# Kernel tuning notes

Hardware: AMD Instinct MI355X
Metric: run time of the kernel (lower is better)

The kernel has to match this reference:

```python
import jax, jax.numpy as jnp
import numpy as np
from jax import lax

B, N_PROP, N_GT = 8, 8000, 256
NUM_CLASSES = 2
IMG_H = IMG_W = 800.0
FG_T = BG_T = 0.5            # Matcher thresholds
WX, WY, WW, WH = 10.0, 10.0, 5.0, 5.0  # BoxCoder weights
SCORE_T, NMS_T = 0.05, 0.5
PRE_NMS, DETS = 1000, 300     # boxes entering NMS, detections_per_img
DW_CLIP = float(np.log(1000.0 / 16.0))


def _rand_boxes(key, shape):
    k1, k2, k3, k4 = jax.random.split(key, 4)
    x1 = jax.random.uniform(k1, shape) * (IMG_W - 60.0)
    y1 = jax.random.uniform(k2, shape) * (IMG_H - 60.0)
    w = 10.0 + jax.random.uniform(k3, shape) * 250.0
    h = 10.0 + jax.random.uniform(k4, shape) * 250.0
    return jnp.stack([x1, y1, jnp.minimum(x1 + w, IMG_W), jnp.minimum(y1 + h, IMG_H)], -1)


def setup_inputs() -> dict:
    key = jax.random.key(0)
    kp, kg, kl, kb = jax.random.split(key, 4)
    n_all = N_PROP + N_GT
    return {
        "proposals": _rand_boxes(kp, (B, N_PROP)),
        "gt_boxes": _rand_boxes(kg, (B, N_GT)),
        "logits": jax.random.normal(kl, (B, n_all, NUM_CLASSES), jnp.float32),
        "box_regression": jax.random.normal(kb, (B, n_all, NUM_CLASSES * 4), jnp.float32) * 0.1,
    }


def box_iou(a, b):
    # a: [Na,4], b: [Nb,4] in xyxy -> [Na,Nb]
    area_a = (a[:, 2] - a[:, 0]) * (a[:, 3] - a[:, 1])
    area_b = (b[:, 2] - b[:, 0]) * (b[:, 3] - b[:, 1])
    lt = jnp.maximum(a[:, None, :2], b[None, :, :2])
    rb = jnp.minimum(a[:, None, 2:], b[None, :, 2:])
    wh = jnp.clip(rb - lt, 0.0)
    inter = wh[..., 0] * wh[..., 1]
    return inter / (area_a[:, None] + area_b[None, :] - inter)


def encode(ref_boxes, gt):
    # BoxCoder.encode, weights (10,10,5,5)
    pw = ref_boxes[:, 2] - ref_boxes[:, 0]
    ph = ref_boxes[:, 3] - ref_boxes[:, 1]
    pcx = ref_boxes[:, 0] + 0.5 * pw
    pcy = ref_boxes[:, 1] + 0.5 * ph
    gw = gt[:, 2] - gt[:, 0]
    gh = gt[:, 3] - gt[:, 1]
    gcx = gt[:, 0] + 0.5 * gw
    gcy = gt[:, 1] + 0.5 * gh
    return jnp.stack([
        WX * (gcx - pcx) / pw,
        WY * (gcy - pcy) / ph,
        WW * jnp.log(gw / pw),
        WH * jnp.log(gh / ph),
    ], -1)


def decode(rel, boxes):
    # rel: [N, C*4], boxes: [N,4] -> [N, C, 4]
    rel = rel.reshape(rel.shape[0], -1, 4)
    pw = boxes[:, 2] - boxes[:, 0]
    ph = boxes[:, 3] - boxes[:, 1]
    pcx = boxes[:, 0] + 0.5 * pw
    pcy = boxes[:, 1] + 0.5 * ph
    dx = rel[..., 0] / WX
    dy = rel[..., 1] / WY
    dw = jnp.minimum(rel[..., 2] / WW, DW_CLIP)
    dh = jnp.minimum(rel[..., 3] / WH, DW_CLIP)
    cx = dx * pw[:, None] + pcx[:, None]
    cy = dy * ph[:, None] + pcy[:, None]
    w = jnp.exp(dw) * pw[:, None]
    h = jnp.exp(dh) * ph[:, None]
    return jnp.stack([cx - 0.5 * w, cy - 0.5 * h, cx + 0.5 * w, cy + 0.5 * h], -1)


def _per_image(prop, gt, logit, breg):
    n_all = prop.shape[0] + gt.shape[0]
    prop_all = jnp.concatenate([prop, gt], 0)  # select_training_samples concat

    # --- assign_targets_to_proposals (Matcher) ---
    iou = box_iou(gt, prop_all)                 # [G, N_all]
    vals = iou.max(0)
    matches = iou.argmax(0)
    # gt_labels are all 1; bg -> 0, between thresholds -> -1 (empty when fg==bg)
    labels = jnp.where(vals < BG_T, 0, jnp.where(vals < FG_T, -1, 1))
    matched_gt = gt[matches]                    # [N_all, 4]
    reg_targets = encode(prop_all, matched_gt)  # [N_all, 4]

    # --- postprocess_detections ---
    pred = decode(breg, prop_all)               # [N_all, C, 4]
    boxes1 = pred[:, 1, :]                      # drop background class
    boxes1 = jnp.stack([
        jnp.clip(boxes1[:, 0], 0.0, IMG_W),
        jnp.clip(boxes1[:, 1], 0.0, IMG_H),
        jnp.clip(boxes1[:, 2], 0.0, IMG_W),
        jnp.clip(boxes1[:, 3], 0.0, IMG_H),
    ], -1)
    scores = jax.nn.softmax(logit, -1)[:, 1]
    sc = jnp.where(scores > SCORE_T, scores, -1.0)  # score_thresh filter

    top_s, top_i = lax.top_k(sc, PRE_NMS)
    top_b = boxes1[top_i]                       # [M, 4]
    ious = box_iou(top_b, top_b)                # [M, M]
    idx = jnp.arange(PRE_NMS)

    def body(keep, i):
        sup = (ious[i] > NMS_T) & keep[i] & (idx > i)
        return keep & ~sup, None

    keep, _ = lax.scan(body, jnp.ones(PRE_NMS, bool), idx)
    final = jnp.where(keep & (top_s > 0.0), top_s, -1.0)
    det_s, sel = lax.top_k(final, DETS)
    det_b = top_b[sel]
    return labels.astype(jnp.float32), reg_targets, det_b, det_s


def reference(proposals, gt_boxes, logits, box_regression):
    return jax.vmap(_per_image)(proposals, gt_boxes, logits, box_regression)
```

## Files before the change

### kernel.cpp

```cpp
#include <hip/hip_runtime.h>
#include <math.h>

#pragma clang fp contract(off)

#define BATCH 8
#define N_PROP 8000
#define N_GT 256
#define N_ALL 8256
#define PRE_NMS 1000
#define DETS 300
#define IMG 800.0f
#define DW_CLIP 4.135166556742356f
#define NWORDS 32
#define NBINS 8192
#define BIN_SCALE 8192.0f
#define PREP_PER_BATCH 65
#define SEL_BLOCKS 8

__device__ __forceinline__ float exf(float x) { return (float)exp((double)x); }
__device__ __forceinline__ float lgf(float x) { return (float)log((double)x); }

__device__ __forceinline__ int score_bin(float s) {
  int b = (int)(s * BIN_SCALE);
  return (b < 0) ? 0 : (b > NBINS - 1 ? NBINS - 1 : b);
}

__device__ __forceinline__ int bxp(int j) { return j ^ ((j >> 5) & 7); }

#define REP32(F) F(0) F(1) F(2) F(3) F(4) F(5) F(6) F(7) F(8) F(9) F(10) \
  F(11) F(12) F(13) F(14) F(15) F(16) F(17) F(18) F(19) F(20) F(21) F(22) \
  F(23) F(24) F(25) F(26) F(27) F(28) F(29) F(30) F(31)


__global__ void __launch_bounds__(1024)
fused_select_prep_kernel(const float* __restrict__ prop,
                         const float* __restrict__ gt,
                         const float* __restrict__ logits,
                         const float* __restrict__ breg,
                         float* __restrict__ out_labels,
                         float* __restrict__ out_regt,
                         float* __restrict__ top_s,
                         float* __restrict__ top_b) {
  const int idx = blockIdx.x;
  const int tid = threadIdx.x;
  __shared__ __align__(16) float ssc[N_ALL];
  __shared__ unsigned hist[NBINS];
  __shared__ __align__(16) float sc2[N_ALL];
  __shared__ unsigned short idx2[N_ALL];
  __shared__ __align__(16) float4 gsh[N_GT];
  __shared__ int s_wt[16], s_wx[16];
  __shared__ int s_T, s_Nc;
  __shared__ __align__(16) float4 gsh4[N_GT];
  __shared__ float s_best[128];
  __shared__ int s_bi[128];

  if (idx < SEL_BLOCKS) {
    const int b = idx;
    const int lane = tid & 63, wid = tid >> 6;

    if (tid < N_GT) gsh[tid] = ((const float4*)(gt + (size_t)b * N_GT * 4))[tid];

    for (int k = tid; k < N_ALL; k += 1024) {
      const float2 lg = *(const float2*)(logits + ((size_t)b * N_ALL + k) * 2);
      const float m = fmaxf(lg.x, lg.y);
      const float e0 = exf(lg.x - m), e1 = exf(lg.y - m);
      const float s = e1 / (e0 + e1);
      ssc[k] = (s > 0.05f) ? s : -1.0f;
    }
    #pragma unroll
    for (int i = 0; i < NBINS / 1024; ++i) hist[tid + i * 1024] = 0u;
    __syncthreads();
    for (int k = tid; k < N_ALL; k += 1024)
      atomicAdd(&hist[score_bin(ssc[k])], 1u);
    __syncthreads();

    int local = 0;
    #pragma unroll
    for (int i = 0; i < NBINS / 1024; ++i) local += (int)hist[tid * (NBINS / 1024) + i];

    int incl = local;
    #pragma unroll
    for (int off = 1; off < 64; off <<= 1) {
      const int u = __shfl_down(incl, off);
      incl += (lane + off < 64) ? u : 0;
    }
    if (lane == 0) s_wt[wid] = incl;
    __syncthreads();
    if (tid < 16) {
      const int v = s_wt[tid];
      int inc2 = v;
      #pragma unroll
      for (int off = 1; off < 16; off <<= 1) {
        const int u = __shfl_down(inc2, off);
        inc2 += (tid + off < 16) ? u : 0;
      }
      s_wx[tid] = inc2 - v;
    }
    __syncthreads();
    const int sa = (incl - local) + s_wx[wid];

    {
      int above = sa;
      const int hi = tid * (NBINS / 1024) + (NBINS / 1024) - 1;
      #pragma unroll
      for (int i = 0; i < NBINS / 1024; ++i) {
        const int bin = hi - i;
        const int c = (int)hist[bin];
        if (above < PRE_NMS && above + c >= PRE_NMS) { s_T = bin; s_Nc = above + c; }
        hist[bin] = (unsigned)above;
        above += c;
      }
    }
    __syncthreads();
    const int T = s_T;
    const int Nc = s_Nc;

    for (int k = tid; k < N_ALL; k += 1024) {
      const float v = ssc[k];
      const int bb = score_bin(v);
      if (bb >= T) {
        const int slot = (int)atomicAdd(&hist[bb], 1u);
        sc2[slot] = v;
        idx2[slot] = (unsigned short)k;
      }
    }
    __syncthreads();

    float* tsb = top_s + (size_t)b * PRE_NMS;
    float4* tbb = (float4*)top_b + (size_t)b * PRE_NMS;
    for (int s = tid; s < Nc; s += 1024) {
      const float my = sc2[s];
      const int myb = score_bin(my);
      const int myi = (int)idx2[s];
      int gl = s;
      while (gl > 0 && score_bin(sc2[gl - 1]) == myb) --gl;
      int rank = gl;
      for (int k2 = gl; k2 < Nc; ++k2) {
        const float v = sc2[k2];
        if (score_bin(v) != myb) break;
        if (k2 == s) continue;
        rank += (int)((v > my) | ((v == my) & ((int)idx2[k2] < myi)));
      }
      if (rank < PRE_NMS) {
        tsb[rank] = my;
        float4 pb;
        if (myi < N_PROP) pb = ((const float4*)(prop + (size_t)b * N_PROP * 4))[myi];
        else              pb = gsh[myi - N_PROP];
        const float pw = pb.z - pb.x, ph = pb.w - pb.y;
        const float pcx = pb.x + 0.5f * pw, pcy = pb.y + 0.5f * ph;
        const float4 r = *(const float4*)(breg + (((size_t)b * N_ALL + myi) * 8 + 4));
        const float dx = r.x / 10.0f, dy = r.y / 10.0f;
        const float dw = fminf(r.z / 5.0f, DW_CLIP);
        const float dh = fminf(r.w / 5.0f, DW_CLIP);
        const float cx = dx * pw + pcx, cy = dy * ph + pcy;
        const float w2 = exf(dw) * pw, h2 = exf(dh) * ph;
        float4 bb;
        bb.x = fminf(fmaxf(cx - 0.5f * w2, 0.0f), IMG);
        bb.y = fminf(fmaxf(cy - 0.5f * h2, 0.0f), IMG);
        bb.z = fminf(fmaxf(cx + 0.5f * w2, 0.0f), IMG);
        bb.w = fminf(fmaxf(cy + 0.5f * h2, 0.0f), IMG);
        tbb[rank] = bb;
      }
    }
  } else {
    const int pbx = idx - SEL_BLOCKS;
    const int b = pbx / PREP_PER_BATCH;
    const int blk = pbx - b * PREP_PER_BATCH;
    {
      if (tid < N_GT)
        gsh4[tid] = ((const float4*)(gt + (size_t)b * N_GT * 4))[tid];
    }
    __syncthreads();

    const int grp = tid >> 3;
    const int gl  = tid & 7;
    const int j0b = blk * 128;
    const int j = j0b + grp;
    const bool jv = (j < N_ALL);

    float x1, y1, x2, y2;
    if (jv && j < N_PROP) {
      const float4 p = ((const float4*)(prop + (size_t)b * N_PROP * 4))[j];
      x1 = p.x; y1 = p.y; x2 = p.z; y2 = p.w;
    } else if (jv) {
      const float4 g = gsh4[j - N_PROP];
      x1 = g.x; y1 = g.y; x2 = g.z; y2 = g.w;
    } else {
      const float4 g = gsh4[0];
      x1 = g.x; y1 = g.y; x2 = g.z; y2 = g.w;
    }
    const float areaP = (x2 - x1) * (y2 - y1);

    float best = -1.0f; int bi = gl;
    #pragma unroll 4
    for (int t = 0; t < 32; ++t) {
      const int i = gl + (t << 3);
      const float4 g = gsh4[i];
      const float ga = (g.z - g.x) * (g.w - g.y);
      const float w = fmaxf(fminf(g.z, x2) - fmaxf(g.x, x1), 0.0f);
      const float h = fmaxf(fminf(g.w, y2) - fmaxf(g.y, y1), 0.0f);
      const float inter = w * h;
      const float iou = inter / (ga + areaP - inter);
      if (iou > best) { best = iou; bi = i; }
    }
    #pragma unroll
    for (int m = 1; m < 8; m <<= 1) {
      const float ov = __shfl_xor(best, m, 64);
      const int   oi = __shfl_xor(bi,  m, 64);
      if (ov > best || (ov == best && oi < bi)) { best = ov; bi = oi; }
    }
    if (gl == 0) { s_best[grp] = best; s_bi[grp] = bi; }
    __syncthreads();

    if (tid < 128) {
      const int j2 = j0b + tid;
      if (j2 < N_ALL) {
        const float bst = s_best[tid];
        const int   gi  = s_bi[tid];

        float px1, py1, px2, py2;
        if (j2 < N_PROP) {
          const float4 p = ((const float4*)(prop + (size_t)b * N_PROP * 4))[j2];
          px1 = p.x; py1 = p.y; px2 = p.z; py2 = p.w;
        } else {
          const float4 g = gsh4[j2 - N_PROP];
          px1 = g.x; py1 = g.y; px2 = g.z; py2 = g.w;
        }

        out_labels[(size_t)b * N_ALL + j2] = (bst < 0.5f) ? 0.0f : 1.0f;

        const float pw = px2 - px1, ph = py2 - py1;
        const float pcx = px1 + 0.5f * pw, pcy = py1 + 0.5f * ph;
        const float4 gb = gsh4[gi];
        const float gw = gb.z - gb.x, gh = gb.w - gb.y;
        const float gcx = gb.x + 0.5f * gw, gcy = gb.y + 0.5f * gh;
        float4 rt;
        rt.x = 10.0f * (gcx - pcx) / pw;
        rt.y = 10.0f * (gcy - pcy) / ph;
        rt.z = 5.0f * lgf(gw / pw);
        rt.w = 5.0f * lgf(gh / ph);
        ((float4*)out_regt)[(size_t)b * N_ALL + j2] = rt;
      }
    }
  }
}

__global__ void mask_kernel(const float* __restrict__ top_b,
                            unsigned* __restrict__ ws_mask) {
  const int b = blockIdx.y;
  __shared__ __align__(16) float4 bx[PRE_NMS];
  const int tid = threadIdx.x;
  {
    const float4* gb = (const float4*)top_b + (size_t)b * PRE_NMS;
    float4 v0 = gb[tid], v1 = gb[tid + 256], v2 = gb[tid + 512];
    float4 v3 = make_float4(0.f, 0.f, 0.f, 0.f);
    const bool g3 = (tid + 768) < PRE_NMS;
    if (g3) v3 = gb[tid + 768];
    bx[bxp(tid)] = v0; bx[bxp(tid + 256)] = v1; bx[bxp(tid + 512)] = v2;
    if (g3) bx[bxp(tid + 768)] = v3;
  }
  __syncthreads();
  const int idx = blockIdx.x * blockDim.x + tid;
  if (idx >= PRE_NMS * NWORDS) return;
  const int i = idx >> 5;
  const int w = idx & 31;
  const float4 bi = bx[bxp(i)];
  const float ai = (bi.z - bi.x) * (bi.w - bi.y);
  unsigned bits = 0u;
  const int j0 = w * 32;
  #pragma unroll 8
  for (int jj = 0; jj < 32; ++jj) {
    const int j = j0 + jj;
    if (j > i && j < PRE_NMS) {
      const float4 bj = bx[bxp(j)];
      const float aj = (bj.z - bj.x) * (bj.w - bj.y);
      const float ww = fmaxf(fminf(bi.z, bj.z) - fmaxf(bi.x, bj.x), 0.0f);
      const float hh = fmaxf(fminf(bi.w, bj.w) - fmaxf(bi.y, bj.y), 0.0f);
      const float inter = ww * hh;
      const float iou = inter / (ai + aj - inter);
      if (iou > 0.5f) bits |= (1u << jj);
    }
  }
  ws_mask[((size_t)b * PRE_NMS + i) * NWORDS + w] = bits;
}

__global__ void __launch_bounds__(256)
scan_kernel(const unsigned* __restrict__ ws_mask,
            const float* __restrict__ top_s,
            const float* __restrict__ top_b,
            float* __restrict__ out_detb,
            float* __restrict__ out_dets) {
  const int b = blockIdx.x;
  const int tid = threadIdx.x;
  __shared__ __align__(16) unsigned smask[PRE_NMS * NWORDS];
  __shared__ int s_npos;
  __shared__ unsigned s_flw[NWORDS];
  __shared__ int s_pref[NWORDS + 1];
  const float* ts = top_s + (size_t)b * PRE_NMS;

  if (tid == 0) s_npos = 0;
  {
    const uint4* gm = (const uint4*)(ws_mask + (size_t)b * PRE_NMS * NWORDS);
    uint4* sm4 = (uint4*)smask;
    #pragma unroll
    for (int gs = 0; gs < 4; ++gs) {
      const int k0 = gs * 2048 + tid;
      uint4 t0 = gm[k0],        t1 = gm[k0 + 256],  t2 = gm[k0 + 512];
      uint4 t3 = gm[k0 + 768],  t4 = gm[k0 + 1024], t5 = gm[k0 + 1280];
      uint4 t6 = gm[k0 + 1536];
      uint4 t7 = make_uint4(0u, 0u, 0u, 0u);
      const bool g7 = (k0 + 1792) < (PRE_NMS * NWORDS / 4);
      if (g7) t7 = gm[k0 + 1792];
      sm4[k0] = t0;        sm4[k0 + 256] = t1;  sm4[k0 + 512] = t2;
      sm4[k0 + 768] = t3;  sm4[k0 + 1024] = t4; sm4[k0 + 1280] = t5;
      sm4[k0 + 1536] = t6;
      if (g7) sm4[k0 + 1792] = t7;
    }
  }
  int cnt = 0;
  for (int k = tid; k < PRE_NMS; k += 256) cnt += (ts[k] > 0.0f) ? 1 : 0;
  __syncthreads();
  if (cnt) atomicAdd(&s_npos, cnt);
  __syncthreads();
  const int n_pos = s_npos;

  unsigned keep = 0u;
  if (tid < 64) {
    const int lane = tid;
    const int lw = lane & 31;
    keep = (lane < NWORDS) ? ((lane == 31) ? 0xFFu : 0xFFFFFFFFu) : 0u;
#define DECLA(J) unsigned rA##J;
    REP32(DECLA)
#undef DECLA
    int c300 = 0;
    for (int win = 0; win < 32; ++win) {
      unsigned sw = (unsigned)__builtin_amdgcn_readlane((int)keep, win);
      if (sw) {
        const int base = win * 32;
#define LOADA(J) rA##J = smask[(base + J) * NWORDS + lw];
        REP32(LOADA)
#undef LOADA
        unsigned sup = 0u;
#define STEPJ(J) { \
        const unsigned mJ = 0u - ((sw >> J) & 1u); \
        const unsigned rwJ = (unsigned)__builtin_amdgcn_readlane((int)rA##J, win); \
        sw &= ~(rwJ & mJ); \
        sup |= (rA##J & mJ); }
        REP32(STEPJ)
#undef STEPJ
        keep &= ~sup;
      }
      int npw = n_pos - win * 32;
      npw = (npw < 0) ? 0 : (npw > 32 ? 32 : npw);
      const unsigned npmw = (npw >= 32) ? 0xFFFFFFFFu : ((1u << npw) - 1u);
      c300 += __popc(sw & npmw);
      if (c300 >= DETS) break;
    }
  }
  __syncthreads();
  if (tid < NWORDS) {
    const int lo = tid * 32;
    int np = n_pos - lo;
    np = (np < 0) ? 0 : (np > 32 ? 32 : np);
    const unsigned npm = (np >= 32) ? 0xFFFFFFFFu : ((1u << np) - 1u);
    s_flw[tid] = keep & npm;
  }
  __syncthreads();
  if (tid == 0) {
    int s = 0;
    #pragma unroll
    for (int w = 0; w < NWORDS; ++w) { s_pref[w] = s; s += __popc(s_flw[w]); }
    s_pref[NWORDS] = s;
  }
  __syncthreads();
  const int tot = s_pref[NWORDS];

  for (int k = tid; k < PRE_NMS; k += 256) {
    const unsigned fw = s_flw[k >> 5];
    const int fbit = (int)((fw >> (k & 31)) & 1u);
    const int pos = s_pref[k >> 5] + __popc(fw & ((1u << (k & 31)) - 1u));
    int slot = -1; float sval = 0.0f;
    if (fbit) {
      if (pos < DETS) { slot = pos; sval = ts[k]; }
    } else {
      const int s2 = tot + (k - pos);
      if (s2 < DETS) { slot = s2; sval = -1.0f; }
    }
    if (slot >= 0) {
      out_dets[(size_t)b * DETS + slot] = sval;
      ((float4*)out_detb)[(size_t)b * DETS + slot] =
          ((const float4*)top_b)[(size_t)b * PRE_NMS + k];
    }
  }
}

extern "C" void kernel_launch(void* const* d_in, const int* in_sizes, int n_in,
                              void* d_out, int out_size, void* d_ws, size_t ws_size,
                              hipStream_t stream) {
  const float* prop   = (const float*)d_in[0];
  const float* gt     = (const float*)d_in[1];
  const float* logits = (const float*)d_in[2];
  const float* breg   = (const float*)d_in[3];

  float* out        = (float*)d_out;
  float* out_labels = out;
  float* out_regt   = out + (size_t)BATCH * N_ALL;
  float* out_detb   = out_regt + (size_t)BATCH * N_ALL * 4;
  float* out_dets   = out_detb + (size_t)BATCH * DETS * 4;

  float* ws_tops   = (float*)d_ws;
  float* ws_topb   = ws_tops + (size_t)BATCH * PRE_NMS;
  unsigned* ws_mask = (unsigned*)(ws_topb + (size_t)BATCH * PRE_NMS * 4);

  hipLaunchKernelGGL(fused_select_prep_kernel,
                     dim3(SEL_BLOCKS + PREP_PER_BATCH * BATCH), dim3(1024), 0, stream,
                     prop, gt, logits, breg, out_labels, out_regt,
                     ws_tops, ws_topb);
  dim3 gridm((PRE_NMS * NWORDS + 255) / 256, BATCH);
  hipLaunchKernelGGL(mask_kernel, gridm, dim3(256), 0, stream,
                     ws_topb, ws_mask);
  hipLaunchKernelGGL(scan_kernel, dim3(BATCH), dim3(256), 0, stream,
                     ws_mask, ws_tops, ws_topb, out_detb, out_dets);
}
```

Baseline: 56.22 us.

## Overlap second half of NMS mask staging with first-half greedy scan

```diff
diff --git a/kernel.cpp b/kernel.cpp
--- a/kernel.cpp
+++ b/kernel.cpp
@@ -62,9 +62,9 @@
 
     for (int k = tid; k < N_ALL; k += 1024) {
       const float2 lg = *(const float2*)(logits + ((size_t)b * N_ALL + k) * 2);
-      const float m = fmaxf(lg.x, lg.y);
-      const float e0 = exf(lg.x - m), e1 = exf(lg.y - m);
-      const float s = e1 / (e0 + e1);
+      const float d = lg.x - lg.y;
+      const float u = exf((d <= 0.0f) ? d : (-d));
+      const float s = (d <= 0.0f) ? (1.0f / (u + 1.0f)) : (u / (1.0f + u));
       ssc[k] = (s > 0.05f) ? s : -1.0f;
     }
     #pragma unroll
@@ -284,6 +284,29 @@
   ws_mask[((size_t)b * PRE_NMS + i) * NWORDS + w] = bits;
 }
 
+#define DECLA(J) unsigned rA##J = 0u;
+#define LOADA(J) rA##J = smask[(base + J) * NWORDS + lw];
+#define STEPJ(J) { \
+  const unsigned mJ = 0u - ((sw >> J) & 1u); \
+  const unsigned rwJ = (unsigned)__builtin_amdgcn_readlane((int)rA##J, win); \
+  sw &= ~(rwJ & mJ); \
+  sup |= (rA##J & mJ); }
+#define SCAN_WIN_BODY { \
+  unsigned sw = (unsigned)__builtin_amdgcn_readlane((int)keep, win); \
+  if (sw) { \
+    const int base = win * 32; \
+    REP32(LOADA) \
+    unsigned sup = 0u; \
+    REP32(STEPJ) \
+    keep &= ~sup; \
+  } \
+  int npw = n_pos - win * 32; \
+  npw = (npw < 0) ? 0 : (npw > 32 ? 32 : npw); \
+  const unsigned npmw = (npw >= 32) ? 0xFFFFFFFFu : ((1u << npw) - 1u); \
+  { const unsigned swf = (unsigned)__builtin_amdgcn_readlane((int)keep, win); \
+    c300 += __popc(swf & npmw); } \
+  if (c300 >= DETS) { done = true; break; } }
+
 __global__ void __launch_bounds__(256)
 scan_kernel(const unsigned* __restrict__ ws_mask,
             const float* __restrict__ top_s,
@@ -297,24 +320,20 @@
   __shared__ unsigned s_flw[NWORDS];
   __shared__ int s_pref[NWORDS + 1];
   const float* ts = top_s + (size_t)b * PRE_NMS;
+  const uint4* gm = (const uint4*)(ws_mask + (size_t)b * PRE_NMS * NWORDS);
+  uint4* sm4 = (uint4*)smask;
 
   if (tid == 0) s_npos = 0;
   {
-    const uint4* gm = (const uint4*)(ws_mask + (size_t)b * PRE_NMS * NWORDS);
-    uint4* sm4 = (uint4*)smask;
-    #pragma unroll
-    for (int gs = 0; gs < 4; ++gs) {
+    #pragma unroll
+    for (int gs = 0; gs < 2; ++gs) {
       const int k0 = gs * 2048 + tid;
       uint4 t0 = gm[k0],        t1 = gm[k0 + 256],  t2 = gm[k0 + 512];
       uint4 t3 = gm[k0 + 768],  t4 = gm[k0 + 1024], t5 = gm[k0 + 1280];
-      uint4 t6 = gm[k0 + 1536];
-      uint4 t7 = make_uint4(0u, 0u, 0u, 0u);
-      const bool g7 = (k0 + 1792) < (PRE_NMS * NWORDS / 4);
-      if (g7) t7 = gm[k0 + 1792];
+      uint4 t6 = gm[k0 + 1536], t7 = gm[k0 + 1792];
       sm4[k0] = t0;        sm4[k0 + 256] = t1;  sm4[k0 + 512] = t2;
       sm4[k0 + 768] = t3;  sm4[k0 + 1024] = t4; sm4[k0 + 1280] = t5;
-      sm4[k0 + 1536] = t6;
-      if (g7) sm4[k0 + 1792] = t7;
+      sm4[k0 + 1536] = t6; sm4[k0 + 1792] = t7;
     }
   }
   int cnt = 0;
@@ -325,37 +344,22 @@
   const int n_pos = s_npos;
 
   unsigned keep = 0u;
+  int c300 = 0;
+  bool done = false;
+  const int lw = tid & 31;
+  REP32(DECLA)
+
   if (tid < 64) {
-    const int lane = tid;
-    const int lw = lane & 31;
-    keep = (lane < NWORDS) ? ((lane == 31) ? 0xFFu : 0xFFFFFFFFu) : 0u;
-#define DECLA(J) unsigned rA##J;
-    REP32(DECLA)
-#undef DECLA
-    int c300 = 0;
-    for (int win = 0; win < 32; ++win) {
-      unsigned sw = (unsigned)__builtin_amdgcn_readlane((int)keep, win);
-      if (sw) {
-        const int base = win * 32;
-#define LOADA(J) rA##J = smask[(base + J) * NWORDS + lw];
-        REP32(LOADA)
-#undef LOADA
-        unsigned sup = 0u;
-#define STEPJ(J) { \
-        const unsigned mJ = 0u - ((sw >> J) & 1u); \
-        const unsigned rwJ = (unsigned)__builtin_amdgcn_readlane((int)rA##J, win); \
-        sw &= ~(rwJ & mJ); \
-        sup |= (rA##J & mJ); }
-        REP32(STEPJ)
-#undef STEPJ
-        keep &= ~sup;
-      }
-      int npw = n_pos - win * 32;
-      npw = (npw < 0) ? 0 : (npw > 32 ? 32 : npw);
-      const unsigned npmw = (npw >= 32) ? 0xFFFFFFFFu : ((1u << npw) - 1u);
-      c300 += __popc(sw & npmw);
-      if (c300 >= DETS) break;
-    }
+    keep = (tid < NWORDS) ? ((tid == 31) ? 0xFFu : 0xFFFFFFFFu) : 0u;
+    for (int win = 0; win < 16; ++win) SCAN_WIN_BODY
+  } else {
+    const int t2 = tid - 64;
+    for (int k = 4096 + t2; k < PRE_NMS * NWORDS / 4; k += 192)
+      sm4[k] = gm[k];
+  }
+  __syncthreads();
+  if (tid < 64 && !done) {
+    for (int win = 16; win < 32; ++win) SCAN_WIN_BODY
   }
   __syncthreads();
   if (tid < NWORDS) {
```

Result: faster. 54.12 us (-3.8%).

## Stream NMS mask rows from global with register double-buffering; simplify softmax

Applied to the files above, without the earlier changes.

```diff
diff --git a/kernel.cpp b/kernel.cpp
--- a/kernel.cpp
+++ b/kernel.cpp
@@ -62,9 +62,9 @@
 
     for (int k = tid; k < N_ALL; k += 1024) {
       const float2 lg = *(const float2*)(logits + ((size_t)b * N_ALL + k) * 2);
-      const float m = fmaxf(lg.x, lg.y);
-      const float e0 = exf(lg.x - m), e1 = exf(lg.y - m);
-      const float s = e1 / (e0 + e1);
+      const float d = lg.x - lg.y;
+      const float u = exf((d <= 0.0f) ? d : (-d));
+      const float s = (d <= 0.0f) ? (1.0f / (u + 1.0f)) : (u / (1.0f + u));
       ssc[k] = (s > 0.05f) ? s : -1.0f;
     }
     #pragma unroll
@@ -284,6 +284,17 @@
   ws_mask[((size_t)b * PRE_NMS + i) * NWORDS + w] = bits;
 }
 
+#define DECLA(J) unsigned rA##J;
+#define DECLN(J) unsigned rN##J;
+#define LOADA0(J) rA##J = gmw[(J) * NWORDS + lw];
+#define LOADN(J) rN##J = gmw[(nb + (J)) * NWORDS + lw];
+#define STEPJ(J) { \
+  const unsigned mJ = 0u - ((sw >> (J)) & 1u); \
+  const unsigned rwJ = (unsigned)__builtin_amdgcn_readlane((int)rA##J, win); \
+  sw &= ~(rwJ & mJ); \
+  sup |= (rA##J & mJ); }
+#define COPYA(J) rA##J = rN##J;
+
 __global__ void __launch_bounds__(256)
 scan_kernel(const unsigned* __restrict__ ws_mask,
             const float* __restrict__ top_s,
@@ -292,31 +303,13 @@
             float* __restrict__ out_dets) {
   const int b = blockIdx.x;
   const int tid = threadIdx.x;
-  __shared__ __align__(16) unsigned smask[PRE_NMS * NWORDS];
   __shared__ int s_npos;
   __shared__ unsigned s_flw[NWORDS];
   __shared__ int s_pref[NWORDS + 1];
   const float* ts = top_s + (size_t)b * PRE_NMS;
+  const unsigned* gmw = ws_mask + (size_t)b * PRE_NMS * NWORDS;
 
   if (tid == 0) s_npos = 0;
-  {
-    const uint4* gm = (const uint4*)(ws_mask + (size_t)b * PRE_NMS * NWORDS);
-    uint4* sm4 = (uint4*)smask;
-    #pragma unroll
-    for (int gs = 0; gs < 4; ++gs) {
-      const int k0 = gs * 2048 + tid;
-      uint4 t0 = gm[k0],        t1 = gm[k0 + 256],  t2 = gm[k0 + 512];
-      uint4 t3 = gm[k0 + 768],  t4 = gm[k0 + 1024], t5 = gm[k0 + 1280];
-      uint4 t6 = gm[k0 + 1536];
-      uint4 t7 = make_uint4(0u, 0u, 0u, 0u);
-      const bool g7 = (k0 + 1792) < (PRE_NMS * NWORDS / 4);
-      if (g7) t7 = gm[k0 + 1792];
-      sm4[k0] = t0;        sm4[k0 + 256] = t1;  sm4[k0 + 512] = t2;
-      sm4[k0 + 768] = t3;  sm4[k0 + 1024] = t4; sm4[k0 + 1280] = t5;
-      sm4[k0 + 1536] = t6;
-      if (g7) sm4[k0 + 1792] = t7;
-    }
-  }
   int cnt = 0;
   for (int k = tid; k < PRE_NMS; k += 256) cnt += (ts[k] > 0.0f) ? 1 : 0;
   __syncthreads();
@@ -326,41 +319,37 @@
 
   unsigned keep = 0u;
   if (tid < 64) {
-    const int lane = tid;
-    const int lw = lane & 31;
-    keep = (lane < NWORDS) ? ((lane == 31) ? 0xFFu : 0xFFFFFFFFu) : 0u;
-#define DECLA(J) unsigned rA##J;
+    const int lw = tid & 31;
+    keep = (tid < NWORDS) ? ((tid == 31) ? 0xFFu : 0xFFFFFFFFu) : 0u;
     REP32(DECLA)
-#undef DECLA
+    REP32(DECLN)
+    REP32(LOADA0)
     int c300 = 0;
     for (int win = 0; win < 32; ++win) {
+      const int nb = ((win + 1) & 31) * 32;
+      REP32(LOADN)
       unsigned sw = (unsigned)__builtin_amdgcn_readlane((int)keep, win);
       if (sw) {
-        const int base = win * 32;
-#define LOADA(J) rA##J = smask[(base + J) * NWORDS + lw];
-        REP32(LOADA)
-#undef LOADA
         unsigned sup = 0u;
-#define STEPJ(J) { \
-        const unsigned mJ = 0u - ((sw >> J) & 1u); \
-        const unsigned rwJ = (unsigned)__builtin_amdgcn_readlane((int)rA##J, win); \
-        sw &= ~(rwJ & mJ); \
-        sup |= (rA##J & mJ); }
         REP32(STEPJ)
-#undef STEPJ
         keep &= ~sup;
       }
       int npw = n_pos - win * 32;
       npw = (npw < 0) ? 0 : (npw > 32 ? 32 : npw);
       const unsigned npmw = (npw >= 32) ? 0xFFFFFFFFu : ((1u << npw) - 1u);
-      c300 += __popc(sw & npmw);
+      {
+        const unsigned swf = (unsigned)__builtin_amdgcn_readlane((int)keep, win);
+        c300 += __popc(swf & npmw);
+      }
       if (c300 >= DETS) break;
-    }
-  }
-  __syncthreads();
+      REP32(COPYA)
+    }
+  }
+  __syncthreads();
+  const int n_pos2 = s_npos;
   if (tid < NWORDS) {
     const int lo = tid * 32;
-    int np = n_pos - lo;
+    int np = n_pos2 - lo;
     np = (np < 0) ? 0 : (np > 32 ? 32 : np);
     const unsigned npm = (np >= 32) ? 0xFFFFFFFFu : ((1u << np) - 1u);
     s_flw[tid] = keep & npm;
```

New measurement: 55.09 us. 2.0% less time.
